# Optimization experiments

Measured on AMD Instinct MI355X. Metric: run time of the kernel, lower is better.

Reference implementation:

```python
import jax, jax.numpy as jnp
import numpy as np
from jax import lax

B = 16   # batch
A = 40   # num_attributes

def _conv(x, w, b, pad):
    y = lax.conv_general_dilated(x, w, (1, 1), [(pad, pad), (pad, pad)],
                                 dimension_numbers=('NCHW', 'OIHW', 'NCHW'))
    return y + b[None, :, None, None]

def _bn_relu(y):
    # BatchNorm2d in training mode; gamma=1, beta=0 (the module's init values)
    m = y.mean(axis=(0, 2, 3), keepdims=True)
    v = ((y - m) ** 2).mean(axis=(0, 2, 3), keepdims=True)
    return jax.nn.relu((y - m) * lax.rsqrt(v + 1e-5))

def _maxpool2(y):
    return lax.reduce_window(y, -jnp.inf, lax.max, (1, 1, 2, 2), (1, 1, 2, 2), 'VALID')

def _gsm(s, t):
    # gumbel_softmax(s, t) == softmax(s / t) along dim 1 (no noise in source)
    return jax.nn.softmax(s / t, axis=1)

def _branch_layer(xb, wa, ba, wb, bb, br, t):
    # xb: [P, B, Cin, H, W]; wa/wb: per-branch conv weights stacked on axis 0
    def one(x, wai, bai, wbi, bbi):
        y = _bn_relu(_conv(x, wai, bai, 1))
        y = _bn_relu(_conv(y, wbi, bbi, 1))
        return _maxpool2(y)
    xs = jax.vmap(one)(xb, wa, ba, wb, bb)       # [P, B, Cout, H/2, W/2]
    # branching_op (training=True): d = softmax(log(softmax(br/0.5)) / t)
    d = _gsm(jnp.log(_gsm(br, 0.5)), float(t))   # [Cnext, P]
    return jnp.einsum('np,pbchw->nbchw', d, xs)  # weighted sum over parents

def reference(x, w10, b10, wa0, ba0, wb0, bb0, wa1, ba1, wb1, bb1,
              wa2, ba2, wb2, bb2, wa3, ba3, wb3, bb3,
              br0, br1, br2, br3, fw1, fb1, fw2, fb2, fw3, fb3, t):
    y = _maxpool2(_bn_relu(_conv(x, w10, b10, 0)))   # conv1_0: [B,64,125,125]
    xb = jnp.stack([y, y])                           # x_branches = [x, x]
    for wa, ba, wb, bb, br in ((wa0, ba0, wb0, bb0, br0),
                               (wa1, ba1, wb1, bb1, br1),
                               (wa2, ba2, wb2, bb2, br2),
                               (wa3, ba3, wb3, bb3, br3)):
        xb = _branch_layer(xb, wa, ba, wb, bb, br, t)
    # xb: [A, B, 32, 7, 7]; AdaptiveAvgPool2d((7,7)) on 7x7 input is identity
    f = xb.reshape(A, B, -1)                          # [A, B, 1568]
    # per-attribute fc1/fc2 heads batched over the attribute axis (dropout omitted)
    h = jax.nn.relu(jnp.einsum('abf,afh->abh', f, fw1) + fb1[:, None, :])
    h = jax.nn.relu(jnp.einsum('abh,ahk->abk', h, fw2) + fb2[:, None, :])
    o = jnp.einsum('abh,ahk->abk', h, fw3) + fb3[:, None, :]   # [A, B, 1]
    return jnp.transpose(o[:, :, 0])                  # cat along dim 1 -> [B, A]

def setup_inputs():
    key = jax.random.key(0)
    ki = iter(jax.random.split(key, 64))
    def rn(shape, s):
        return jax.random.normal(next(ki), shape, jnp.float32) * s
    inp = {'x': jax.random.normal(next(ki), (B, 3, 256, 256), jnp.float32)}
    inp['w10'] = rn((64, 3, 7, 7), 0.1)
    inp['b10'] = jnp.zeros((64,), jnp.float32)
    P = [2, 4, 8, 16]       # parents per branch layer
    cout = [64, 64, 64, 32] # num_in_channels[layer+1]
    for L in range(4):
        inp['wa%d' % L] = rn((P[L], 64, 64, 3, 3), 0.06)
        inp['ba%d' % L] = jnp.zeros((P[L], 64), jnp.float32)
        inp['wb%d' % L] = rn((P[L], cout[L], 64, 3, 3), 0.06)
        inp['bb%d' % L] = jnp.zeros((P[L], cout[L]), jnp.float32)
    C = [4, 8, 16, A]       # children per branch layer
    for L in range(4):
        inp['br%d' % L] = jax.random.uniform(next(ki), (C[L], P[L]), dtype=jnp.float32)
    inp['fw1'] = rn((A, 1568, 128), 0.01)
    inp['fb1'] = jnp.zeros((A, 128), jnp.float32)
    inp['fw2'] = rn((A, 128, 128), 0.01)
    inp['fb2'] = jnp.zeros((A, 128), jnp.float32)
    inp['fw3'] = rn((A, 128, 1), 0.01)
    inp['fb3'] = jnp.zeros((A, 1), jnp.float32)
    inp['t'] = 10
    return inp
```

## Files before the change

### kernel.cpp

```cpp
#include <hip/hip_runtime.h>
#include <math.h>

#define DIVUP(a,b) (((a)+(b)-1)/(b))

typedef _Float16 f16x8 __attribute__((ext_vector_type(8)));
typedef _Float16 f16x4 __attribute__((ext_vector_type(4)));
typedef float    f32x4 __attribute__((ext_vector_type(4)));

#define LBAR() do { asm volatile("s_waitcnt lgkmcnt(0)" ::: "memory"); \
                    __builtin_amdgcn_s_barrier(); } while (0)

template<int POOL, int C1, int HinP, int WinP, int Hout, int Wout, int Cout,
         int M, int NITER, int H2, int W2, int H2c, int W2c>
__global__ __launch_bounds__(256, 4) void conv_mfma(
    const _Float16* __restrict__ in, long inZstride,
    const _Float16* __restrict__ wt,
    _Float16* __restrict__ out, long outZstride, float2* __restrict__ part)
{
    __shared__ __align__(16) char smem[10240];
    float2* red = (float2*)smem;

    int bx;
    {
        int n = gridDim.x, orig = blockIdx.x;
        int q = n >> 3, r = n & 7;
        int xcd = orig & 7, idx = orig >> 3;
        bx = (xcd < r ? xcd * (q + 1) : r * (q + 1) + (xcd - r) * q) + idx;
    }

    const int tid  = threadIdx.x;
    const int wv   = tid >> 6;
    const int ln15 = tid & 15;
    const int lhi  = (tid >> 4) & 3;
    const int sn   = tid & 63;
    const int skb  = tid >> 6;
    const int sdst = sn * 40 + skb * 8;

    const _Float16* ip = in + (size_t)blockIdx.z * inZstride;

    auto pixbase = [&](int mA) -> int {
        int nb, h, w; bool valid;
        if (POOL) {
            int r = mA & 3, quad = mA >> 2;
            const int cpi = H2c * W2c;
            nb = quad / cpi;
            int rem = quad - nb * cpi;
            int h2 = rem / W2c, w2 = rem - h2 * W2c;
            h = h2 * 2 + (r >> 1); w = w2 * 2 + (r & 1);
            valid = (mA < M) && (h < Hout) && (w < Wout);
        } else {
            const int HW = Hout * Wout;
            valid = mA < M;
            int mm = valid ? mA : 0;
            nb = mm / HW;
            int rem = mm - nb * HW;
            h = rem / Wout; w = rem - h * Wout;
        }
        if (!valid) { nb = 0; h = 0; w = 0; }
        if (C1) return ((nb * 256 + h) * 256 + w) * 4;
        return ((nb * HinP + h) * WinP + w) * 64;
    };
    auto rowvalid = [&](int mA) -> bool {
        if (POOL) {
            int r = mA & 3, quad = mA >> 2;
            const int cpi = H2c * W2c;
            int nb = quad / cpi;
            int rem = quad - nb * cpi;
            int h2 = rem / W2c, w2 = rem - h2 * W2c;
            int h = h2 * 2 + (r >> 1), w = w2 * 2 + (r & 1);
            return (mA < M) && (h < Hout) && (w < Wout);
        }
        return mA < M;
    };

    int abase[2];
#pragma unroll
    for (int q = 0; q < 2; ++q)
        abase[q] = pixbase(bx * 128 + wv * 32 + q * 16 + ln15);

    unsigned vmask = 0;
#pragma unroll
    for (int q = 0; q < 2; ++q)
#pragma unroll
        for (int r = 0; r < 4; ++r)
            vmask |= (unsigned)rowvalid(bx * 128 + wv * 32 + q * 16 + lhi * 4 + r)
                     << (q * 4 + r);

    const _Float16* wp = wt + (size_t)blockIdx.z * NITER * 2048;

    auto loadA = [&](int it, f16x8 (&a)[2]) {
        int off;
        if (C1) off = it * 1024 + lhi * 8;
        else { int tap = it >> 1; int kh = tap / 3, kw = tap - 3 * kh;
               off = (kh * WinP + kw) * 64 + (it & 1) * 32 + lhi * 8; }
#pragma unroll
        for (int q = 0; q < 2; ++q)
            a[q] = *(const f16x8*)(ip + abase[q] + off);
    };

    f32x4 acc[2][4] = {};
    f16x8 a0[2], a1[2], a2[2];
    f16x8 sb;

    {
        f16x8 h = *(const f16x8*)(wp + (size_t)(skb * 64 + sn) * 8);
        *(f16x8*)((_Float16*)smem + sdst) = h;
        loadA(0, a0);
        if (NITER > 1) {
            loadA(1, a1);
            sb = *(const f16x8*)(wp + (size_t)((4 + skb) * 64 + sn) * 8);
        }
        if (NITER > 2) loadA(2, a2);
        LBAR();
    }

#define REGION(IT, CUR, AR)                                                       \
    {                                                                             \
        const int itc = (IT);                                                     \
        if (itc + 1 < NITER)                                                      \
            *(f16x8*)((_Float16*)(smem + ((CUR) ^ 1) * 5120) + sdst) = sb;        \
        const _Float16* rb = (const _Float16*)(smem + (CUR) * 5120);              \
        f16x8 bf[4];                                                              \
        _Pragma("unroll")                                                         \
        for (int t = 0; t < 4; ++t)                                               \
            bf[t] = *(const f16x8*)(rb + (t * 16 + ln15) * 40 + lhi * 8);         \
        if (itc + 2 < NITER)                                                      \
            sb = *(const f16x8*)(wp +                                             \
                     (size_t)(((itc + 2) * 4 + skb) * 64 + sn) * 8);              \
        _Pragma("unroll")                                                         \
        for (int t = 0; t < 4; ++t)                                               \
            _Pragma("unroll")                                                     \
            for (int q = 0; q < 2; ++q)                                           \
                acc[q][t] = __builtin_amdgcn_mfma_f32_16x16x32_f16(AR[q], bf[t], acc[q][t], 0, 0, 0); \
        if (itc + 3 < NITER) loadA(itc + 3, AR);                                  \
        LBAR();                                                                   \
    }

    for (int it = 0; it < NITER; it += 6) {
        REGION(it, 0, a0);
        if (it + 1 < NITER) REGION(it + 1, 1, a1);
        if (it + 2 < NITER) REGION(it + 2, 0, a2);
        if (it + 3 < NITER) REGION(it + 3, 1, a0);
        if (it + 4 < NITER) REGION(it + 4, 0, a1);
        if (it + 5 < NITER) REGION(it + 5, 1, a2);
    }
#undef REGION

#pragma unroll
    for (int t = 0; t < 4; ++t) {
        float s = 0.f, s2 = 0.f;
#pragma unroll
        for (int q = 0; q < 2; ++q)
#pragma unroll
            for (int r = 0; r < 4; ++r) {
                float v = ((vmask >> (q * 4 + r)) & 1u) ? acc[q][t][r] : 0.f;
                s += v; s2 += v * v;
            }
        red[(ln15 + 16 * t) * 17 + (wv * 4 + lhi)] = make_float2(s, s2);
    }
    __syncthreads();
    if (tid < 64) {
        float s = 0.f, s2 = 0.f;
#pragma unroll
        for (int q = 0; q < 16; ++q) { float2 v = red[tid * 17 + q]; s += v.x; s2 += v.y; }
        part[((size_t)blockIdx.z * 64 + tid) * gridDim.x + bx] = make_float2(s, s2);
    }

    _Float16* zout = out + (size_t)blockIdx.z * outZstride;
#pragma unroll
    for (int q = 0; q < 2; ++q) {
        const int mbase = bx * 128 + wv * 32 + q * 16 + lhi * 4;
        if (POOL) {
            if (mbase < M) {
                int quad = mbase >> 2;
                const int cpi = H2c * W2c;
                int nb2  = quad / cpi;
                int rem  = quad - nb2 * cpi;
                int h2 = rem / W2c, w2 = rem - h2 * W2c;
                if (h2 < H2 && w2 < W2) {
                    _Float16* op = zout + ((size_t)(nb2 * H2 + h2) * W2 + w2) * Cout;
#pragma unroll
                    for (int t = 0; t < 4; ++t) {
                        int n = ln15 + 16 * t;
                        if (n < Cout) {
                            float mx = fmaxf(fmaxf(acc[q][t][0], acc[q][t][1]),
                                             fmaxf(acc[q][t][2], acc[q][t][3]));
                            op[n] = (_Float16)mx;
                        }
                    }
                }
            }
        } else {
#pragma unroll
            for (int r = 0; r < 4; ++r) {
                int m = mbase + r;
                if (m < M) {
                    _Float16* op = zout + (size_t)m * Cout;
#pragma unroll
                    for (int t = 0; t < 4; ++t) {
                        int n = ln15 + 16 * t;
                        if (n < Cout) op[n] = (_Float16)acc[q][t][r];
                    }
                }
            }
        }
    }
}

__global__ __launch_bounds__(256) void bn_finalize(const float2* __restrict__ part,
                                                   int nblkx, double Ninv,
                                                   float2* __restrict__ stats)
{
    __shared__ double sh[512];
    const int zc = blockIdx.x, tid = threadIdx.x;
    const float2* p = part + (size_t)zc * nblkx;
    double s = 0, s2 = 0;
    for (int i = tid; i < nblkx; i += 256) { s += p[i].x; s2 += p[i].y; }
    sh[tid] = s; sh[256 + tid] = s2;
    __syncthreads();
    for (int st = 128; st > 0; st >>= 1) {
        if (tid < st) { sh[tid] += sh[tid + st]; sh[256 + tid] += sh[256 + tid + st]; }
        __syncthreads();
    }
    if (tid == 0) {
        float mean = (float)(sh[0] * Ninv);
        float var  = (float)(sh[256] * Ninv - (double)mean * (double)mean);
        if (var < 0.f) var = 0.f;
        stats[zc] = make_float2(mean, rsqrtf(var + 1e-5f));
    }
}

__global__ void bn_split(const _Float16* __restrict__ raw, const float2* __restrict__ stats,
                         _Float16* __restrict__ outF, int H, int W, int total)
{
    int idx = blockIdx.x * 256 + threadIdx.x;
    if (idx >= total) return;
    const int Hp = H + 2, Wp = W + 2;
    int c4 = idx & 15;
    int t  = idx >> 4;
    int wp = t % Wp; t /= Wp;
    int hp = t % Hp; int img = t / Hp;
    size_t o = (((size_t)img * Hp + hp) * Wp + wp) * 64 + c4 * 4;
    f16x4 hi;
    if (hp == 0 || hp == Hp - 1 || wp == 0 || wp == Wp - 1) {
#pragma unroll
        for (int j = 0; j < 4; ++j) hi[j] = (_Float16)0.f;
    } else {
        f16x4 v = *(const f16x4*)(raw + (((size_t)img * H + (hp - 1)) * W + (wp - 1)) * 64 + c4 * 4);
        const float2* st = stats + (img >> 4) * 64 + c4 * 4;
#pragma unroll
        for (int j = 0; j < 4; ++j) {
            float2 s = st[j];
            hi[j] = (_Float16)fmaxf(((float)v[j] - s.x) * s.y, 0.f);
        }
    }
    *(f16x4*)(outF + o) = hi;
}

__global__ void mix_split(const _Float16* __restrict__ pooled, const float2* __restrict__ stats,
                          const float* __restrict__ d, _Float16* __restrict__ outF,
                          int H, int W, int P, long strideP, int total)
{
    int idx = blockIdx.x * 256 + threadIdx.x;
    if (idx >= total) return;
    const int Hp = H + 2, Wp = W + 2;
    int c4 = idx & 15;
    int t  = idx >> 4;
    int wp = t % Wp; t /= Wp;
    int hp = t % Hp; t /= Hp;
    int n  = t & 15;
    int cc = t >> 4;
    size_t o = (((size_t)(cc * 16 + n) * Hp + hp) * Wp + wp) * 64 + c4 * 4;
    f16x4 hi;
    if (hp == 0 || hp == Hp - 1 || wp == 0 || wp == Wp - 1) {
#pragma unroll
        for (int j = 0; j < 4; ++j) hi[j] = (_Float16)0.f;
    } else {
        float a[4] = {0.f, 0.f, 0.f, 0.f};
        const _Float16* pb = pooled + (((size_t)n * H + (hp - 1)) * W + (wp - 1)) * 64 + c4 * 4;
        for (int p = 0; p < P; ++p) {
            f16x4 v = *(const f16x4*)(pb + (size_t)p * strideP);
            const float2* st = stats + p * 64 + c4 * 4;
            float dc = d[cc * P + p];
#pragma unroll
            for (int j = 0; j < 4; ++j) {
                float2 s = st[j];
                a[j] = fmaf(dc, fmaxf(((float)v[j] - s.x) * s.y, 0.f), a[j]);
            }
        }
#pragma unroll
        for (int j = 0; j < 4; ++j) hi[j] = (_Float16)a[j];
    }
    *(f16x4*)(outF + o) = hi;
}

__global__ void mix_last(const _Float16* __restrict__ pooled, const float2* __restrict__ stats,
                         const float* __restrict__ d, float* __restrict__ out, int total)
{
    int idx = blockIdx.x * 256 + threadIdx.x;
    if (idx >= total) return;
    int c  = idx & 31;
    int t  = idx >> 5;
    int hw = t % 49; t /= 49;
    int n  = t & 15;
    int a  = t >> 4;
    float acc = 0.f;
    const _Float16* pb = pooled + ((size_t)n * 49 + hw) * 32 + c;
    for (int p = 0; p < 16; ++p) {
        float2 s = stats[p * 64 + c];
        acc = fmaf(d[a * 16 + p], fmaxf(((float)pb[(size_t)p * 25088] - s.x) * s.y, 0.f), acc);
    }
    out[idx] = acc;
}

__global__ void prep_x(const float* __restrict__ x, _Float16* __restrict__ xF)
{
    int idx = blockIdx.x * 256 + threadIdx.x;
    if (idx >= 16 * 65536) return;
    int n = idx >> 16, hw = idx & 65535;
    f16x4 hi;
#pragma unroll
    for (int ci = 0; ci < 3; ++ci)
        hi[ci] = (_Float16)x[((size_t)n * 3 + ci) * 65536 + hw];
    hi[3] = (_Float16)0.f;
    *(f16x4*)(xF + (size_t)idx * 4) = hi;
}

__global__ void wtrans1(const float* __restrict__ w, _Float16* __restrict__ wt)
{
    int i = blockIdx.x * 256 + threadIdx.x;
    if (i >= 28 * 512) return;
    int j = i & 7, n = (i >> 3) & 63, kb = i >> 9;
    int k = kb * 8 + j;
    int kh = k >> 5, r = k & 31, kw = r >> 2, ci = r & 3;
    float v = (kw < 7 && ci < 3) ? w[((n * 3 + ci) * 7 + kh) * 7 + kw] : 0.f;
    wt[i] = (_Float16)v;
}

__global__ void wtrans3(const float* __restrict__ w, _Float16* __restrict__ wt,
                        int P, int Cout)
{
    int total = P * 72 * 512;
    for (int i = blockIdx.x * 256 + threadIdx.x; i < total; i += gridDim.x * 256) {
        int j = i & 7, n = (i >> 3) & 63, kb = (i >> 9) % 72, p = (i >> 9) / 72;
        int k = kb * 8 + j;
        int ci = k & 63, tap = k >> 6, kh = tap / 3, kw = tap - 3 * kh;
        float v = (n < Cout) ? w[(((size_t)(p * Cout + n)) * 64 + ci) * 9 + kh * 3 + kw] : 0.f;
        wt[i] = (_Float16)v;
    }
}

__global__ void dcalc(const float* __restrict__ br0, const float* __restrict__ br1,
                      const float* __restrict__ br2, const float* __restrict__ br3,
                      const void* __restrict__ tptr, float* __restrict__ D)
{
    const int L = blockIdx.x;
    const float* br; int C, P, off;
    if      (L == 0) { br = br0; C = 4;  P = 2;  off = 0;   }
    else if (L == 1) { br = br1; C = 8;  P = 4;  off = 8;   }
    else if (L == 2) { br = br2; C = 16; P = 8;  off = 40;  }
    else             { br = br3; C = 40; P = 16; off = 168; }
    int ti = *(const int*)tptr;
    float t = (ti > 0 && ti < 1000000) ? (float)ti : *(const float*)tptr;
    const int c = threadIdx.x;
    if (c >= C) return;
    float u[16];
    float mx = -1e30f;
#pragma unroll
    for (int p = 0; p < 16; ++p) if (p < P) { u[p] = br[c * P + p] * 2.0f; mx = fmaxf(mx, u[p]); }
    float se = 0.f;
#pragma unroll
    for (int p = 0; p < 16; ++p) if (p < P) se += expf(u[p] - mx);
    float lse = mx + logf(se);
    float mx2 = -1e30f;
#pragma unroll
    for (int p = 0; p < 16; ++p) if (p < P) { u[p] = (u[p] - lse) / t; mx2 = fmaxf(mx2, u[p]); }
    float se2 = 0.f;
#pragma unroll
    for (int p = 0; p < 16; ++p) if (p < P) { u[p] = expf(u[p] - mx2); se2 += u[p]; }
#pragma unroll
    for (int p = 0; p < 16; ++p) if (p < P) D[off + c * P + p] = u[p] / se2;
}

__global__ __launch_bounds__(128) void fc1_k(const float* __restrict__ f,
                                             const float* __restrict__ w1,
                                             const float* __restrict__ b1,
                                             float* __restrict__ h1)
{
    const int a = blockIdx.x >> 4;
    const int b = blockIdx.x & 15;
    const int i = threadIdx.x;
    const float* fv = f + ((size_t)a * 16 + b) * 1568;
    const float* wv = w1 + (size_t)a * 1568 * 128 + i;
    float acc = b1[a * 128 + i];
    for (int hw = 0; hw < 49; ++hw)
        for (int c = 0; c < 32; ++c)
            acc = fmaf(fv[hw * 32 + c], wv[(size_t)(c * 49 + hw) * 128], acc);
    h1[((size_t)a * 16 + b) * 128 + i] = fmaxf(acc, 0.f);
}

__global__ __launch_bounds__(128) void fc23_k(const float* __restrict__ h1,
                                              const float* __restrict__ w2,
                                              const float* __restrict__ b2,
                                              const float* __restrict__ w3,
                                              const float* __restrict__ b3,
                                              float* __restrict__ out)
{
    __shared__ float sh1[16][128];
    __shared__ float sh2[16][128];
    const int a = blockIdx.x;
    const int i = threadIdx.x;
    for (int b = 0; b < 16; ++b) sh1[b][i] = h1[((size_t)a * 16 + b) * 128 + i];
    __syncthreads();
    float acc[16];
#pragma unroll
    for (int b = 0; b < 16; ++b) acc[b] = b2[a * 128 + i];
    for (int ff = 0; ff < 128; ++ff) {
        float wv = w2[((size_t)a * 128 + ff) * 128 + i];
#pragma unroll
        for (int b = 0; b < 16; ++b) acc[b] = fmaf(sh1[b][ff], wv, acc[b]);
    }
    for (int b = 0; b < 16; ++b) sh2[b][i] = fmaxf(acc[b], 0.f);
    __syncthreads();
    if (i < 16) {
        float o = b3[a];
        for (int ff = 0; ff < 128; ++ff) o = fmaf(sh2[i][ff], w3[a * 128 + ff], o);
        out[i * 40 + a] = o;
    }
}

extern "C" void kernel_launch(void* const* d_in, const int* in_sizes, int n_in,
                              void* d_out, int out_size, void* d_ws, size_t ws_size,
                              hipStream_t stream)
{
    (void)in_sizes; (void)n_in;

    const float* x   = (const float*)d_in[0];
    const float* w10 = (const float*)d_in[1];
    const float* wa[4] = {(const float*)d_in[3],  (const float*)d_in[7],
                          (const float*)d_in[11], (const float*)d_in[15]};
    const float* wb[4] = {(const float*)d_in[5],  (const float*)d_in[9],
                          (const float*)d_in[13], (const float*)d_in[17]};
    const float* br[4] = {(const float*)d_in[19], (const float*)d_in[20],
                          (const float*)d_in[21], (const float*)d_in[22]};
    const float* fw1 = (const float*)d_in[23];
    const float* fb1 = (const float*)d_in[24];
    const float* fw2 = (const float*)d_in[25];
    const float* fb2 = (const float*)d_in[26];
    const float* fw3 = (const float*)d_in[27];
    const float* fb3 = (const float*)d_in[28];
    float* out = (float*)d_out;

    const int Pl[4]  = {2, 4, 8, 16};
    const int CBs[4] = {64, 64, 64, 32};

    const size_t NEED = 47000000ull * 4ull;
    if (ws_size < NEED) {
        hipMemsetAsync(d_out, 0, (size_t)out_size * sizeof(float), stream);
        return;
    }
    float* ws = (float*)d_ws;
    size_t o = 0;
    _Float16* WT1 = (_Float16*)(ws + o); o += 7168;
    _Float16 *WTA[4], *WTB[4];
    for (int L = 0; L < 4; ++L) {
        WTA[L] = (_Float16*)(ws + o); o += (size_t)Pl[L] * 18432;
        WTB[L] = (_Float16*)(ws + o); o += (size_t)Pl[L] * 18432;
    }
    float*  D     = ws + o; o += 1024;
    float2* STATS = (float2*)(ws + o); o += 4352;
    float2* STATS_C1 = STATS;
    float2* STATS_A  = STATS + 64;
    float2* STATS_B  = STATS + 1088;
    float*  H1 = ws + o; o += 81920;
    float*  A6 = ws + o; o += 524288;
    float*  A5 = ws + o; o += 4000000;
    float*  A4 = ws + o; o += 16000000;
    float*  A3 = ws + o; o += 16600000;
    float*  A2 = ws + o; o += 8400000;

    float2* PART   = (float2*)A6;
    float2* PARTC1 = (float2*)A5;
    _Float16* xcF = (_Float16*)A3;
    _Float16* A2F = (_Float16*)A2;
    _Float16* A3F = (_Float16*)A3;
    _Float16* A4F = (_Float16*)A4;
    _Float16* A5F = (_Float16*)A5;

    prep_x<<<4096, 256, 0, stream>>>(x, xcF);
    wtrans1<<<56, 256, 0, stream>>>(w10, WT1);
    for (int L = 0; L < 4; ++L) {
        int tA = Pl[L] * 72 * 512;
        wtrans3<<<DIVUP(tA, 256), 256, 0, stream>>>(wa[L], WTA[L], Pl[L], 64);
        wtrans3<<<DIVUP(tA, 256), 256, 0, stream>>>(wb[L], WTB[L], Pl[L], CBs[L]);
    }
    dcalc<<<4, 64, 0, stream>>>(br[0], br[1], br[2], br[3], d_in[29], D);

    conv_mfma<1, 1, 256, 256, 250, 250, 64, 1000000, 7, 125, 125, 125, 125>
        <<<dim3(7813, 1, 1), 256, 0, stream>>>(xcF, 0, WT1, A4F, 0, PARTC1);
    bn_finalize<<<64, 256, 0, stream>>>(PARTC1, 7813, 1.0 / 1000000.0, STATS_C1);
    bn_split<<<DIVUP(16 * 127 * 127 * 16, 256), 256, 0, stream>>>(
        A4F, STATS_C1, A2F, 125, 125, 16 * 127 * 127 * 16);

    conv_mfma<0, 0, 127, 127, 125, 125, 64, 250000, 18, 0, 0, 1, 1>
        <<<dim3(1954, 1, 2), 256, 0, stream>>>(
            A2F, 0, WTA[0], A4F, 16000000, PART);
    bn_finalize<<<128, 256, 0, stream>>>(PART, 1954, 1.0 / 250000.0, STATS_A);
    bn_split<<<DIVUP(2 * 16 * 127 * 127 * 16, 256), 256, 0, stream>>>(
        A4F, STATS_A, A3F, 125, 125, 2 * 16 * 127 * 127 * 16);
    conv_mfma<1, 0, 127, 127, 125, 125, 64, 254016, 18, 62, 62, 63, 63>
        <<<dim3(1985, 1, 2), 256, 0, stream>>>(
            A3F, 16516096, WTB[0], A5F, 3936256, PART);
    bn_finalize<<<128, 256, 0, stream>>>(PART, 1985, 1.0 / 250000.0, STATS_B);
    mix_split<<<DIVUP(4 * 16 * 64 * 64 * 16, 256), 256, 0, stream>>>(
        A5F, STATS_B, D + 0, A2F, 62, 62, 2, 3936256, 4 * 16 * 64 * 64 * 16);

    conv_mfma<0, 0, 64, 64, 62, 62, 64, 61504, 18, 0, 0, 1, 1>
        <<<dim3(481, 1, 4), 256, 0, stream>>>(
            A2F, 4194304, WTA[1], A4F, 3936256, PART);
    bn_finalize<<<256, 256, 0, stream>>>(PART, 481, 1.0 / 61504.0, STATS_A);
    bn_split<<<DIVUP(64 * 64 * 64 * 16, 256), 256, 0, stream>>>(
        A4F, STATS_A, A3F, 62, 62, 64 * 64 * 64 * 16);
    conv_mfma<1, 0, 64, 64, 62, 62, 64, 61504, 18, 31, 31, 31, 31>
        <<<dim3(481, 1, 4), 256, 0, stream>>>(
            A3F, 4194304, WTB[1], A5F, 984064, PART);
    bn_finalize<<<256, 256, 0, stream>>>(PART, 481, 1.0 / 61504.0, STATS_B);
    mix_split<<<DIVUP(8 * 16 * 33 * 33 * 16, 256), 256, 0, stream>>>(
        A5F, STATS_B, D + 8, A2F, 31, 31, 4, 984064, 8 * 16 * 33 * 33 * 16);

    conv_mfma<0, 0, 33, 33, 31, 31, 64, 15376, 18, 0, 0, 1, 1>
        <<<dim3(121, 1, 8), 256, 0, stream>>>(
            A2F, 1115136, WTA[2], A4F, 984064, PART);
    bn_finalize<<<512, 256, 0, stream>>>(PART, 121, 1.0 / 15376.0, STATS_A);
    bn_split<<<DIVUP(128 * 33 * 33 * 16, 256), 256, 0, stream>>>(
        A4F, STATS_A, A3F, 31, 31, 128 * 33 * 33 * 16);
    conv_mfma<1, 0, 33, 33, 31, 31, 64, 16384, 18, 15, 15, 16, 16>
        <<<dim3(128, 1, 8), 256, 0, stream>>>(
            A3F, 1115136, WTB[2], A5F, 230400, PART);
    bn_finalize<<<512, 256, 0, stream>>>(PART, 128, 1.0 / 15376.0, STATS_B);
    mix_split<<<DIVUP(16 * 16 * 17 * 17 * 16, 256), 256, 0, stream>>>(
        A5F, STATS_B, D + 40, A2F, 15, 15, 8, 230400, 16 * 16 * 17 * 17 * 16);

    conv_mfma<0, 0, 17, 17, 15, 15, 64, 3600, 18, 0, 0, 1, 1>
        <<<dim3(29, 1, 16), 256, 0, stream>>>(
            A2F, 295936, WTA[3], A4F, 230400, PART);
    bn_finalize<<<1024, 256, 0, stream>>>(PART, 29, 1.0 / 3600.0, STATS_A);
    bn_split<<<DIVUP(256 * 17 * 17 * 16, 256), 256, 0, stream>>>(
        A4F, STATS_A, A3F, 15, 15, 256 * 17 * 17 * 16);
    conv_mfma<1, 0, 17, 17, 15, 15, 32, 4096, 18, 7, 7, 8, 8>
        <<<dim3(32, 1, 16), 256, 0, stream>>>(
            A3F, 295936, WTB[3], A5F, 25088, PART);
    bn_finalize<<<1024, 256, 0, stream>>>(PART, 32, 1.0 / 3600.0, STATS_B);
    mix_last<<<DIVUP(40 * 16 * 49 * 32, 256), 256, 0, stream>>>(
        A5F, STATS_B, D + 168, A2, 40 * 16 * 49 * 32);

    fc1_k<<<640, 128, 0, stream>>>(A2, fw1, fb1, H1);
    fc23_k<<<40, 128, 0, stream>>>(H1, fw2, fb2, fw3, fb3, out);
}
```

Measured before the change: 639.3 us.

## Load conv weights directly from global into registers, dropping LDS staging and barriers

The MFMA conv kernel no longer stages the weight (B) fragments through double-buffered shared memory with a barrier every iteration. Each lane now loads its four B fragments straight from global memory, relying on cache since all waves read the same weights. The pipeline becomes a simple two-stage register double buffer for A and B. This removes the LDS writes, LDS reads and per-iteration block barriers, at the cost of four times more global/L2 weight traffic and higher register use, which may reduce occupancy.

```diff
diff --git a/kernel.cpp b/kernel.cpp
--- a/kernel.cpp
+++ b/kernel.cpp
@@ -6,9 +6,6 @@
 typedef _Float16 f16x8 __attribute__((ext_vector_type(8)));
 typedef _Float16 f16x4 __attribute__((ext_vector_type(4)));
 typedef float    f32x4 __attribute__((ext_vector_type(4)));
-
-#define LBAR() do { asm volatile("s_waitcnt lgkmcnt(0)" ::: "memory"); \
-                    __builtin_amdgcn_s_barrier(); } while (0)
 
 template<int POOL, int C1, int HinP, int WinP, int Hout, int Wout, int Cout,
          int M, int NITER, int H2, int W2, int H2c, int W2c>
@@ -17,8 +14,7 @@
     const _Float16* __restrict__ wt,
     _Float16* __restrict__ out, long outZstride, float2* __restrict__ part)
 {
-    __shared__ __align__(16) char smem[10240];
-    float2* red = (float2*)smem;
+    __shared__ __align__(16) float2 red[64 * 17];
 
     int bx;
     {
@@ -32,9 +28,6 @@
     const int wv   = tid >> 6;
     const int ln15 = tid & 15;
     const int lhi  = (tid >> 4) & 3;
-    const int sn   = tid & 63;
-    const int skb  = tid >> 6;
-    const int sdst = sn * 40 + skb * 8;
 
     const _Float16* ip = in + (size_t)blockIdx.z * inZstride;
 
@@ -87,6 +80,7 @@
                      << (q * 4 + r);
 
     const _Float16* wp = wt + (size_t)blockIdx.z * NITER * 2048;
+    const _Float16* wlane = wp + (size_t)(lhi * 64 + ln15) * 8;
 
     auto loadA = [&](int it, f16x8 (&a)[2]) {
         int off;
@@ -97,54 +91,33 @@
         for (int q = 0; q < 2; ++q)
             a[q] = *(const f16x8*)(ip + abase[q] + off);
     };
+    auto loadB = [&](int it, f16x8 (&b)[4]) {
+        const _Float16* base = wlane + (size_t)it * 2048;
+#pragma unroll
+        for (int t = 0; t < 4; ++t)
+            b[t] = *(const f16x8*)(base + t * 128);
+    };
 
     f32x4 acc[2][4] = {};
-    f16x8 a0[2], a1[2], a2[2];
-    f16x8 sb;
-
-    {
-        f16x8 h = *(const f16x8*)(wp + (size_t)(skb * 64 + sn) * 8);
-        *(f16x8*)((_Float16*)smem + sdst) = h;
-        loadA(0, a0);
-        if (NITER > 1) {
-            loadA(1, a1);
-            sb = *(const f16x8*)(wp + (size_t)((4 + skb) * 64 + sn) * 8);
+    f16x8 aC[2], bC[4], aN[2], bN[4];
+
+    loadA(0, aC); loadB(0, bC);
+    for (int it = 0; it < NITER; it += 2) {
+        if (it + 1 < NITER) { loadA(it + 1, aN); loadB(it + 1, bN); }
+#pragma unroll
+        for (int t = 0; t < 4; ++t)
+#pragma unroll
+            for (int q = 0; q < 2; ++q)
+                acc[q][t] = __builtin_amdgcn_mfma_f32_16x16x32_f16(aC[q], bC[t], acc[q][t], 0, 0, 0);
+        if (it + 2 < NITER) { loadA(it + 2, aC); loadB(it + 2, bC); }
+        if (it + 1 < NITER) {
+#pragma unroll
+            for (int t = 0; t < 4; ++t)
+#pragma unroll
+                for (int q = 0; q < 2; ++q)
+                    acc[q][t] = __builtin_amdgcn_mfma_f32_16x16x32_f16(aN[q], bN[t], acc[q][t], 0, 0, 0);
         }
-        if (NITER > 2) loadA(2, a2);
-        LBAR();
-    }
-
-#define REGION(IT, CUR, AR)                                                       \
-    {                                                                             \
-        const int itc = (IT);                                                     \
-        if (itc + 1 < NITER)                                                      \
-            *(f16x8*)((_Float16*)(smem + ((CUR) ^ 1) * 5120) + sdst) = sb;        \
-        const _Float16* rb = (const _Float16*)(smem + (CUR) * 5120);              \
-        f16x8 bf[4];                                                              \
-        _Pragma("unroll")                                                         \
-        for (int t = 0; t < 4; ++t)                                               \
-            bf[t] = *(const f16x8*)(rb + (t * 16 + ln15) * 40 + lhi * 8);         \
-        if (itc + 2 < NITER)                                                      \
-            sb = *(const f16x8*)(wp +                                             \
-                     (size_t)(((itc + 2) * 4 + skb) * 64 + sn) * 8);              \
-        _Pragma("unroll")                                                         \
-        for (int t = 0; t < 4; ++t)                                               \
-            _Pragma("unroll")                                                     \
-            for (int q = 0; q < 2; ++q)                                           \
-                acc[q][t] = __builtin_amdgcn_mfma_f32_16x16x32_f16(AR[q], bf[t], acc[q][t], 0, 0, 0); \
-        if (itc + 3 < NITER) loadA(itc + 3, AR);                                  \
-        LBAR();                                                                   \
-    }
-
-    for (int it = 0; it < NITER; it += 6) {
-        REGION(it, 0, a0);
-        if (it + 1 < NITER) REGION(it + 1, 1, a1);
-        if (it + 2 < NITER) REGION(it + 2, 0, a2);
-        if (it + 3 < NITER) REGION(it + 3, 1, a0);
-        if (it + 4 < NITER) REGION(it + 4, 0, a1);
-        if (it + 5 < NITER) REGION(it + 5, 1, a2);
-    }
-#undef REGION
+    }
 
 #pragma unroll
     for (int t = 0; t < 4; ++t) {
```

Result: slower. 741.2 us (+15.9%).
